# Kernel tuning notes

Measured on AMD Instinct MI355X. Metric: run time of the kernel, lower is better.

Reference implementation:

```python
import jax, jax.numpy as jnp
import numpy as np

H, B, T = 4, 16, 4000
E, D, A, C, K, O = 512, 512, 128, 10, 101, 512


def setup_inputs() -> dict:
    key = jax.random.key(0)
    ks = jax.random.split(key, 12)
    return {
        "enc_pad": jax.random.normal(ks[0], (B, T, E), jnp.float32),
        "enc_len": jax.random.randint(ks[1], (B,), T // 2, T + 1, jnp.int32),
        "dec_z": jax.random.normal(ks[2], (B, D), jnp.float32),
        "att_prev": jax.random.uniform(ks[3], (H, B, T), jnp.float32) / T,
        # learned parameters (per-head stacks)
        "Wenc": jax.random.normal(ks[4], (H, E, A), jnp.float32) / np.sqrt(E).astype(np.float32),
        "benc": jnp.zeros((H, A), jnp.float32),
        "Wdec": jax.random.normal(ks[5], (H, D, A), jnp.float32) / np.sqrt(D).astype(np.float32),
        "Watt": jax.random.normal(ks[6], (H, C, A), jnp.float32) / np.sqrt(C).astype(np.float32),
        "conv_w": jax.random.normal(ks[7], (H, C, K), jnp.float32) / np.sqrt(K).astype(np.float32),
        "gv": jax.random.normal(ks[8], (H, A), jnp.float32) / np.sqrt(A).astype(np.float32),
        "Wo": jax.random.normal(ks[9], (H * E, O), jnp.float32) / np.sqrt(H * E).astype(np.float32),
        "bo": jnp.zeros((O,), jnp.float32),
    }


def reference(enc_pad, enc_len, dec_z, att_prev, Wenc, benc, Wdec, Watt, conv_w, gv, Wo, bo):
    scaling = 1.0
    Hh, Bb, Tt = att_prev.shape
    Cc, Kk = conv_w.shape[1], conv_w.shape[2]
    pad_l = Kk // 2
    pad_r = Kk // 2 if Kk % 2 == 1 else Kk // 2 - 1
    # location conv: grouped 1D conv over heads. lhs [B,H,Tp], rhs [H*C,1,K]
    x = jnp.pad(att_prev.transpose(1, 0, 2), ((0, 0), (0, 0), (pad_l, pad_r)))
    rhs = conv_w.reshape(Hh * Cc, 1, Kk)
    conv = jax.lax.conv_general_dilated(
        x, rhs, window_strides=(1,), padding='VALID',
        dimension_numbers=('NCH', 'OIH', 'NCH'), feature_group_count=Hh)  # [B,H*C,T]
    conv = conv.reshape(Bb, Hh, Cc, Tt)
    att_conv = jnp.einsum('bhct,hca->bhta', conv, Watt)                    # mlp_att
    enc_proj = jnp.einsum('bte,hea->bhta', enc_pad, Wenc) + benc[None, :, None, :]  # mlp_enc
    dec_proj = jnp.einsum('bd,hda->bha', dec_z, Wdec)[:, :, None, :]       # mlp_dec
    e = jnp.einsum('bhta,ha->bht', jnp.tanh(enc_proj + dec_proj + att_conv), gv)  # gvec
    w = jax.nn.softmax(scaling * e, axis=-1)                               # [B,H,T]
    c = jnp.einsum('bht,bte->bhe', w, enc_pad).reshape(Bb, Hh * enc_pad.shape[-1])
    out = c @ Wo + bo                                                      # mlp_o
    return out, w.transpose(1, 0, 2)  # ws stacked as [H,B,T]
```

## Files before the change

kernel.cpp:

```cpp
#include <hip/hip_runtime.h>
#include <hip/hip_bf16.h>

#define H_ 4
#define B_ 16
#define T_ 4000
#define E_ 512
#define D_ 512
#define A_ 128
#define C_ 10
#define K_ 101
#define O_ 512
#define TC_ 50
#define CH_ (T_ / TC_)

typedef __attribute__((ext_vector_type(4))) float f32x4;
typedef __attribute__((ext_vector_type(8)))  short short8;

#define MFMA16(a, b, c) __builtin_amdgcn_mfma_f32_16x16x32_bf16(a, b, c, 0, 0, 0)

#define GLL16(gp, lp) __builtin_amdgcn_global_load_lds( \
    (const __attribute__((address_space(1))) unsigned int*)(gp), \
    (__attribute__((address_space(3))) unsigned int*)(lp), 16, 0, 0)

static __device__ __forceinline__ unsigned short f2bf(float x) {
  unsigned u = __float_as_uint(x);
  unsigned r = (u + 0x7FFFu + ((u >> 16) & 1u)) >> 16;
  return (unsigned short)r;
}
static __device__ __forceinline__ unsigned pk2(float a, float b) {
  return (unsigned)f2bf(a) | ((unsigned)f2bf(b) << 16);
}
static __device__ __forceinline__ unsigned cvtpk(float lo, float hi) {
  unsigned r;
  asm("v_cvt_pk_bf16_f32 %0, %1, %2" : "=v"(r) : "v"(lo), "v"(hi));
  return r;
}
static __device__ __forceinline__ uint4 packbf8(float4 f0, float4 f1) {
  uint4 u;
  u.x = cvtpk(f0.x, f0.y); u.y = cvtpk(f0.z, f0.w);
  u.z = cvtpk(f1.x, f1.y); u.w = cvtpk(f1.z, f1.w);
  return u;
}
static __device__ __forceinline__ float tanh_fast(float x) {
  return 1.0f - 2.0f / (__expf(2.0f * x) + 1.0f);
}
static __device__ __forceinline__ int swz(int r) {
  return (r & 3) ^ ((r >> 2) & 3);
}

__global__ __launch_bounds__(256) void k_prep(const float* __restrict__ Wenc,
                                              const float* __restrict__ Watt,
                                              const float* __restrict__ dec_z,
                                              const float* __restrict__ Wdec,
                                              const float* __restrict__ benc,
                                              char* __restrict__ wbs2,
                                              char* __restrict__ wattb2,
                                              float* __restrict__ addv4) {
  const int bid = blockIdx.x;
  const int tid = threadIdx.x;
  if (bid < 128) {
    const int c = bid * 256 + tid;
    const int kt = c >> 11;
    const int ci = c & 2047;
    const int col = ci >> 2, cc = ci & 3;
    const int h = col >> 7, a = col & 127;
    const int kk = kt * 32 + ((cc ^ swz(col)) & 3) * 8;
    const float* w = Wenc + ((size_t)h * E_ + kk) * A_ + a;
    uint4 u;
    u.x = pk2(w[0], w[A_]);
    u.y = pk2(w[2 * A_], w[3 * A_]);
    u.z = pk2(w[4 * A_], w[5 * A_]);
    u.w = pk2(w[6 * A_], w[7 * A_]);
    ((uint4*)wbs2)[c] = u;
  } else if (bid == 128) {
#pragma unroll
    for (int q = 0; q < 4; ++q) {
      const int cw = q * 256 + tid;
      const int h = cw >> 8;
      const int rr = cw & 255;
      const int col = rr >> 1, half = rr & 1;
      unsigned short v[8];
#pragma unroll
      for (int j = 0; j < 8; ++j) {
        const int k = half * 8 + j;
        v[j] = (k < C_) ? f2bf(Watt[((size_t)h * C_ + k) * A_ + col]) : (unsigned short)0;
      }
      uint4 u;
      u.x = (unsigned)v[0] | ((unsigned)v[1] << 16);
      u.y = (unsigned)v[2] | ((unsigned)v[3] << 16);
      u.z = (unsigned)v[4] | ((unsigned)v[5] << 16);
      u.w = (unsigned)v[6] | ((unsigned)v[7] << 16);
      ((uint4*)wattb2)[cw] = u;
    }
  } else {
    const int idx = bid - 129;
    const int b = idx >> 3, h = (idx >> 1) & 3, ks = idx & 1;
    const int a = tid & 127, kh = tid >> 7;
    const int p = ks * 2 + kh;
    const int d0 = p * 128;
    const float* z = dec_z + (size_t)b * D_ + d0;
    const float* w = Wdec + ((size_t)h * D_ + d0) * A_ + a;
    float s = (p == 0) ? benc[h * A_ + a] : 0.f;
#pragma unroll 8
    for (int d = 0; d < 128; ++d) s += z[d] * w[(size_t)d * A_];
    addv4[(((size_t)p * B_ + b) * H_ + h) * A_ + a] = s;
  }
}

__global__ __launch_bounds__(256) void k_conv(const float* __restrict__ att_prev,
                                              const float* __restrict__ conv_w,
                                              char* __restrict__ convpad) {
  const int bh = blockIdx.x;
  const int b = bh / H_, h = bh % H_;
  const int t0 = blockIdx.y * 256;
  __shared__ float ap[256 + K_ - 1 + 3];
  __shared__ float cw[C_ * K_];
  const float* src = att_prev + ((size_t)h * B_ + b) * T_;
  for (int i = threadIdx.x; i < 256 + K_ - 1; i += 256) {
    int tt = t0 - (K_ / 2) + i;
    ap[i] = (tt >= 0 && tt < T_) ? src[tt] : 0.f;
  }
  for (int i = threadIdx.x; i < C_ * K_; i += 256) cw[i] = conv_w[(size_t)h * C_ * K_ + i];
  __syncthreads();
  const int t = t0 + threadIdx.x;
  if (t < T_) {
    float s[C_];
#pragma unroll
    for (int c = 0; c < C_; ++c) s[c] = 0.f;
    for (int k = 0; k < K_; ++k) {
      float apv = ap[threadIdx.x + k];
#pragma unroll
      for (int c = 0; c < C_; ++c) s[c] += cw[c * K_ + k] * apv;
    }
    uint4 u0, u1;
    u0.x = pk2(s[0], s[1]); u0.y = pk2(s[2], s[3]);
    u0.z = pk2(s[4], s[5]); u0.w = pk2(s[6], s[7]);
    u1.x = pk2(s[8], s[9]); u1.y = 0u; u1.z = 0u; u1.w = 0u;
    char* dst = convpad + (size_t)(b * T_ + t) * 128 + h * 32;
    *(uint4*)dst = u0;
    *(uint4*)(dst + 16) = u1;
  }
}

__global__ __launch_bounds__(512, 4) void k_fused_e_mfma(
    const float* __restrict__ enc,
    const char*  __restrict__ wbs2,
    const char*  __restrict__ convpad,
    const char*  __restrict__ wattb2,
    const float* __restrict__ addv4,
    const float* __restrict__ gv,
    float* __restrict__ e_out) {
  __shared__ char smem[73728];
  const int tid = threadIdx.x;
  const int wv = tid >> 6;
  const int lane = tid & 63, l15 = lane & 15, lg = lane >> 4;
  const int m0 = blockIdx.x * 64;
  const int h = wv >> 1;
  const bool aRole = (wv < 4);

  f32x4 acc[4][4];
#pragma unroll
  for (int i = 0; i < 4; ++i)
#pragma unroll
    for (int j = 0; j < 4; ++j) acc[i][j] = (f32x4){0.f, 0.f, 0.f, 0.f};

  int aOff[4], bOff[4];
#pragma unroll
  for (int q = 0; q < 4; ++q) {
    const int row = q * 16 + l15;
    aOff[q] = row * 64 + (((lg ^ swz(row)) & 3) << 4);
    const int col = wv * 64 + q * 16 + l15;
    bOff[q] = col * 64 + (((lg ^ swz(col)) & 3) << 4);
  }

  const int arow = tid >> 2, ac = tid & 3;
  const int ks = ((ac ^ swz(arow)) & 3) * 8;
  const float* eR = enc + (size_t)(m0 + arow) * E_ + ks;
  const int wOff = arow * 64 + ac * 16;
  const char* bsrc = wbs2 + (size_t)(wv - 4) * 8192 + lane * 16;
  char* bdstBase = smem + 8192 + (wv - 4) * 8192;

  float4 X0, X1;

  if (aRole) {
    float4 c0 = *(const float4*)eR;
    float4 c1 = *(const float4*)(eR + 4);
    X0 = *(const float4*)(eR + 32);
    X1 = *(const float4*)(eR + 36);
    *(uint4*)(smem + wOff) = packbf8(c0, c1);
    asm volatile("s_waitcnt vmcnt(2) lgkmcnt(0)" ::: "memory");
  } else {
#pragma unroll
    for (int i = 0; i < 8; ++i)
      GLL16(bsrc + i * 1024, bdstBase + i * 1024);
    asm volatile("s_waitcnt vmcnt(0) lgkmcnt(0)" ::: "memory");
  }
  __builtin_amdgcn_sched_barrier(0);
  __builtin_amdgcn_s_barrier();

#pragma unroll 1
  for (int kt = 0; kt < 16; ++kt) {
    const int cur = kt & 1;
    const char* bufA = smem + cur * 4096;
    const char* bufB = smem + 8192 + cur * 32768;

    if (!aRole && kt < 15) {
      const char* s = bsrc + (size_t)(kt + 1) * 32768;
      char* d = smem + 8192 + (cur ^ 1) * 32768 + (wv - 4) * 8192;
#pragma unroll
      for (int i = 0; i < 8; ++i)
        GLL16(s + i * 1024, d + i * 1024);
    }
    __builtin_amdgcn_sched_barrier(0);

    short8 aF[4];
#pragma unroll
    for (int q = 0; q < 4; ++q) aF[q] = *(const short8*)(bufA + aOff[q]);
#pragma unroll
    for (int qn = 0; qn < 4; ++qn) {
      short8 bF = *(const short8*)(bufB + bOff[qn]);
#pragma unroll
      for (int qm = 0; qm < 4; ++qm)
        acc[qm][qn] = MFMA16(aF[qm], bF, acc[qm][qn]);
    }

    if (aRole) {
      if (kt < 15)
        *(uint4*)(smem + (cur ^ 1) * 4096 + wOff) = packbf8(X0, X1);
      if (kt < 14) {
        X0 = *(const float4*)(eR + (kt + 2) * 32);
        X1 = *(const float4*)(eR + (kt + 2) * 32 + 4);
      }
    }

    if (kt < 14) {
      if (aRole)
        asm volatile("s_waitcnt vmcnt(2) lgkmcnt(0)" ::: "memory");
      else
        asm volatile("s_waitcnt vmcnt(0) lgkmcnt(0)" ::: "memory");
    } else {
      asm volatile("s_waitcnt vmcnt(0) lgkmcnt(0)" ::: "memory");
    }
    __builtin_amdgcn_sched_barrier(0);
    __builtin_amdgcn_s_barrier();
  }

  {
    short8 zf;
#pragma unroll
    for (int i = 0; i < 8; ++i) zf[i] = 0;
    short8 cf[4], wf[4];
#pragma unroll
    for (int q = 0; q < 4; ++q) { cf[q] = zf; wf[q] = zf; }
    if (lg < 2) {
#pragma unroll
      for (int q = 0; q < 4; ++q) {
        const int row = m0 + q * 16 + l15;
        cf[q] = *(const short8*)(convpad + (size_t)row * 128 + h * 32 + lg * 16);
        const int col = (wv & 1) * 64 + q * 16 + l15;
        wf[q] = *(const short8*)(wattb2 + ((size_t)h * 128 + col) * 32 + lg * 16);
      }
    }
#pragma unroll
    for (int qm = 0; qm < 4; ++qm)
#pragma unroll
      for (int qn = 0; qn < 4; ++qn)
        acc[qm][qn] = MFMA16(cf[qm], wf[qn], acc[qm][qn]);
  }

  {
    const unsigned b0w = (unsigned)m0 / 4000u;
    const unsigned b1w = (unsigned)(m0 + 63) / 4000u;
    float av0[4], av1[4], gvr[4];
#pragma unroll
    for (int qn = 0; qn < 4; ++qn) {
      const int col = (wv & 1) * 64 + qn * 16 + l15;
      const int i0 = (int)b0w * 512 + h * 128 + col;
      const int i1 = (int)b1w * 512 + h * 128 + col;
      av0[qn] = addv4[i0] + addv4[8192 + i0] + addv4[16384 + i0] + addv4[24576 + i0];
      av1[qn] = addv4[i1] + addv4[8192 + i1] + addv4[16384 + i1] + addv4[24576 + i1];
      gvr[qn] = gv[h * 128 + col];
    }
    float* Pb = (float*)smem;
#pragma unroll
    for (int qm = 0; qm < 4; ++qm) {
#pragma unroll
      for (int r = 0; r < 4; ++r) {
        const int rowLocal = qm * 16 + lg * 4 + r;
        const unsigned brow = (unsigned)(m0 + rowLocal);
        const unsigned bb = brow / 4000u;
        const int sel = (bb != b0w);
        float s = 0.f;
#pragma unroll
        for (int qn = 0; qn < 4; ++qn)
          s += gvr[qn] * tanh_fast(acc[qm][qn][r] + (sel ? av1[qn] : av0[qn]));
        s += __shfl_xor(s, 1);
        s += __shfl_xor(s, 2);
        s += __shfl_xor(s, 4);
        s += __shfl_xor(s, 8);
        if (l15 == 0) Pb[wv * 64 + rowLocal] = s;
      }
    }
  }
  __syncthreads();
  if (tid < 256) {
    const float* Pb = (const float*)smem;
    const int hh = tid >> 6, r = tid & 63;
    const float ev = Pb[(hh * 2) * 64 + r] + Pb[(hh * 2 + 1) * 64 + r];
    const unsigned brow = (unsigned)(m0 + r);
    const unsigned bb = brow / 4000u;
    const unsigned tt = brow - bb * 4000u;
    e_out[((size_t)bb * H_ + hh) * T_ + tt] = ev;
  }
}

__global__ __launch_bounds__(256) void k_msum(const float* __restrict__ e_in,
                                              float2* __restrict__ msum) {
  const int bh = blockIdx.x;
  const float* er = e_in + (size_t)bh * T_;
  __shared__ float red[256];
  const int tid = threadIdx.x;
  float m = -1e30f;
  for (int t = tid; t < T_; t += 256) m = fmaxf(m, er[t]);
  red[tid] = m;
  __syncthreads();
  for (int s = 128; s > 0; s >>= 1) {
    if (tid < s) red[tid] = fmaxf(red[tid], red[tid + s]);
    __syncthreads();
  }
  m = red[0];
  __syncthreads();
  float sum = 0.f;
  for (int t = tid; t < T_; t += 256) sum += __expf(er[t] - m);
  red[tid] = sum;
  __syncthreads();
  for (int s = 128; s > 0; s >>= 1) {
    if (tid < s) red[tid] += red[tid + s];
    __syncthreads();
  }
  if (tid == 0) msum[bh] = make_float2(m, 1.0f / red[0]);
}

__global__ __launch_bounds__(128) void k_ctx(const float* __restrict__ enc,
                                             const float* __restrict__ e_in,
                                             const float2* __restrict__ msum,
                                             float* __restrict__ wout,
                                             float* __restrict__ partial) {
  const int b = blockIdx.x, tc = blockIdx.y;
  const int t0 = tc * CH_;
  const int tid = threadIdx.x;
  __shared__ float wls[H_ * CH_];
  for (int i = tid; i < H_ * CH_; i += 128) {
    const int h = i / CH_, tt = i - h * CH_;
    const float2 ms = msum[b * H_ + h];
    const float w = __expf(e_in[((size_t)b * H_ + h) * T_ + t0 + tt] - ms.x) * ms.y;
    wls[i] = w;
    wout[((size_t)h * B_ + b) * T_ + t0 + tt] = w;
  }
  __syncthreads();
  float4 a0 = {0,0,0,0}, a1 = {0,0,0,0}, a2 = {0,0,0,0}, a3 = {0,0,0,0};
  const float4* enc4 = (const float4*)enc;
  const size_t ebase = ((size_t)b * T_ + t0) * 128 + tid;
#pragma unroll 8
  for (int tt = 0; tt < CH_; ++tt) {
    const float4 x = enc4[ebase + (size_t)tt * 128];
    const float w0 = wls[tt], w1 = wls[CH_ + tt], w2 = wls[2 * CH_ + tt], w3 = wls[3 * CH_ + tt];
    a0.x += w0 * x.x; a0.y += w0 * x.y; a0.z += w0 * x.z; a0.w += w0 * x.w;
    a1.x += w1 * x.x; a1.y += w1 * x.y; a1.z += w1 * x.z; a1.w += w1 * x.w;
    a2.x += w2 * x.x; a2.y += w2 * x.y; a2.z += w2 * x.z; a2.w += w2 * x.w;
    a3.x += w3 * x.x; a3.y += w3 * x.y; a3.z += w3 * x.z; a3.w += w3 * x.w;
  }
  float4* p4 = (float4*)partial;
  const size_t pbase = (((size_t)tc * B_ + b) * H_) * 128 + tid;
  p4[pbase] = a0;
  p4[pbase + 128] = a1;
  p4[pbase + 256] = a2;
  p4[pbase + 384] = a3;
}

__global__ __launch_bounds__(256) void k_out_part(const float* __restrict__ partial,
                                                  const float* __restrict__ Wo,
                                                  float* __restrict__ p2) {
  const int b = blockIdx.x;
  const int o = blockIdx.y * 256 + threadIdx.x;
  const int kc = blockIdx.z;
  __shared__ float cS[256];
  const int he0 = kc * 256;
  {
    float s = 0.f;
#pragma unroll
    for (int tc = 0; tc < TC_; ++tc)
      s += partial[((size_t)tc * B_ + b) * (H_ * E_) + he0 + threadIdx.x];
    cS[threadIdx.x] = s;
  }
  __syncthreads();
  float s = 0.f;
#pragma unroll 8
  for (int i = 0; i < 256; ++i) s += cS[i] * Wo[(size_t)(he0 + i) * O_ + o];
  p2[((size_t)kc * B_ + b) * O_ + o] = s;
}

__global__ __launch_bounds__(512) void k_out_fin(const float* __restrict__ p2,
                                                 const float* __restrict__ bo,
                                                 float* __restrict__ out) {
  const int b = blockIdx.x, o = threadIdx.x;
  float s = bo[o];
#pragma unroll
  for (int kc = 0; kc < 8; ++kc) s += p2[((size_t)kc * B_ + b) * O_ + o];
  out[b * O_ + o] = s;
}

extern "C" void kernel_launch(void* const* d_in, const int* in_sizes, int n_in,
                              void* d_out, int out_size, void* d_ws, size_t ws_size,
                              hipStream_t stream) {
  (void)in_sizes; (void)n_in; (void)out_size; (void)ws_size;
  const float* enc      = (const float*)d_in[0];
  const float* dec_z    = (const float*)d_in[2];
  const float* att_prev = (const float*)d_in[3];
  const float* Wenc     = (const float*)d_in[4];
  const float* benc     = (const float*)d_in[5];
  const float* Wdec     = (const float*)d_in[6];
  const float* Watt     = (const float*)d_in[7];
  const float* conv_w   = (const float*)d_in[8];
  const float* gv       = (const float*)d_in[9];
  const float* Wo       = (const float*)d_in[10];
  const float* bo       = (const float*)d_in[11];

  float* out  = (float*)d_out;
  float* wout = out + B_ * O_;

  char* wsb = (char*)d_ws;
  float*  e_buf   = (float*)(wsb);
  char*   convpad = wsb + 1024000;
  char*   wbs2    = wsb + 9216000;
  char*   wattb2  = wsb + 9740288;
  float*  addv4   = (float*)(wsb + 9756672);
  float2* msum    = (float2*)(wsb + 9887744);
  float*  partial = (float*)(wsb + 9888256);
  float*  p2      = (float*)(wsb + 16441856);

  hipLaunchKernelGGL(k_prep, dim3(257), dim3(256), 0, stream,
                     Wenc, Watt, dec_z, Wdec, benc, wbs2, wattb2, addv4);
  hipLaunchKernelGGL(k_conv, dim3(B_ * H_, 16), dim3(256), 0, stream, att_prev, conv_w, convpad);
  hipLaunchKernelGGL(k_fused_e_mfma, dim3(1000), dim3(512), 0, stream,
                     enc, wbs2, convpad, wattb2, addv4, gv, e_buf);
  hipLaunchKernelGGL(k_msum, dim3(B_ * H_), dim3(256), 0, stream, e_buf, msum);
  hipLaunchKernelGGL(k_ctx, dim3(B_, TC_), dim3(128), 0, stream, enc, e_buf, msum, wout, partial);
  hipLaunchKernelGGL(k_out_part, dim3(B_, O_ / 256, 8), dim3(256), 0, stream, partial, Wo, p2);
  hipLaunchKernelGGL(k_out_fin, dim3(B_), dim3(512), 0, stream, p2, bo, out);
}
```

Baseline: 143.2 us.

## Split k_ctx time chunk across four warps, add MFMA priority and pointer increments

k_ctx now launches 512 threads per block. Four groups of 128 each cover 20 of the 80 timesteps in the chunk, and their accumulators are combined through shared memory before the partial is written. The aim is more loads in flight and better occupancy on the bandwidth-bound context pass over enc. The MFMA GEMM loop also gains s_setprio around its MFMA block and replaces recomputed prefetch addresses with incremented pointers. The cost is a shared-memory reduction and an extra barrier in k_ctx.

```diff
diff --git a/kernel.cpp b/kernel.cpp
--- a/kernel.cpp
+++ b/kernel.cpp
@@ -181,6 +181,8 @@
   char* bdstBase = smem + 8192 + (wv - 4) * 8192;
 
   float4 X0, X1;
+  const float* eP = eR + 64;
+  const char* bsP = bsrc + 32768;
 
   if (aRole) {
     float4 c0 = *(const float4*)eR;
@@ -205,17 +207,17 @@
     const char* bufB = smem + 8192 + cur * 32768;
 
     if (!aRole && kt < 15) {
-      const char* s = bsrc + (size_t)(kt + 1) * 32768;
       char* d = smem + 8192 + (cur ^ 1) * 32768 + (wv - 4) * 8192;
 #pragma unroll
       for (int i = 0; i < 8; ++i)
-        GLL16(s + i * 1024, d + i * 1024);
+        GLL16(bsP + i * 1024, d + i * 1024);
     }
     __builtin_amdgcn_sched_barrier(0);
 
     short8 aF[4];
 #pragma unroll
     for (int q = 0; q < 4; ++q) aF[q] = *(const short8*)(bufA + aOff[q]);
+    __builtin_amdgcn_s_setprio(1);
 #pragma unroll
     for (int qn = 0; qn < 4; ++qn) {
       short8 bF = *(const short8*)(bufB + bOff[qn]);
@@ -223,14 +225,18 @@
       for (int qm = 0; qm < 4; ++qm)
         acc[qm][qn] = MFMA16(aF[qm], bF, acc[qm][qn]);
     }
+    __builtin_amdgcn_s_setprio(0);
 
     if (aRole) {
       if (kt < 15)
         *(uint4*)(smem + (cur ^ 1) * 4096 + wOff) = packbf8(X0, X1);
       if (kt < 14) {
-        X0 = *(const float4*)(eR + (kt + 2) * 32);
-        X1 = *(const float4*)(eR + (kt + 2) * 32 + 4);
+        X0 = *(const float4*)eP;
+        X1 = *(const float4*)(eP + 4);
+        eP += 32;
       }
+    } else {
+      bsP += 32768;
     }
 
     if (kt < 14) {
@@ -341,7 +347,7 @@
   if (tid == 0) msum[bh] = make_float2(m, 1.0f / red[0]);
 }
 
-__global__ __launch_bounds__(128) void k_ctx(const float* __restrict__ enc,
+__global__ __launch_bounds__(512) void k_ctx(const float* __restrict__ enc,
                                              const float* __restrict__ e_in,
                                              const float2* __restrict__ msum,
                                              float* __restrict__ wout,
@@ -349,8 +355,10 @@
   const int b = blockIdx.x, tc = blockIdx.y;
   const int t0 = tc * CH_;
   const int tid = threadIdx.x;
+  const int grp = tid >> 7, lt = tid & 127;
   __shared__ float wls[H_ * CH_];
-  for (int i = tid; i < H_ * CH_; i += 128) {
+  __shared__ float4 red[3][4][128];
+  for (int i = tid; i < H_ * CH_; i += 512) {
     const int h = i / CH_, tt = i - h * CH_;
     const float2 ms = msum[b * H_ + h];
     const float w = __expf(e_in[((size_t)b * H_ + h) * T_ + t0 + tt] - ms.x) * ms.y;
@@ -360,22 +368,44 @@
   __syncthreads();
   float4 a0 = {0,0,0,0}, a1 = {0,0,0,0}, a2 = {0,0,0,0}, a3 = {0,0,0,0};
   const float4* enc4 = (const float4*)enc;
-  const size_t ebase = ((size_t)b * T_ + t0) * 128 + tid;
-#pragma unroll 8
-  for (int tt = 0; tt < CH_; ++tt) {
+  const int tg = grp * 20;
+  const size_t ebase = ((size_t)b * T_ + t0 + tg) * 128 + lt;
+#pragma unroll 5
+  for (int tt = 0; tt < 20; ++tt) {
     const float4 x = enc4[ebase + (size_t)tt * 128];
-    const float w0 = wls[tt], w1 = wls[CH_ + tt], w2 = wls[2 * CH_ + tt], w3 = wls[3 * CH_ + tt];
+    const float w0 = wls[tg + tt];
+    const float w1 = wls[CH_ + tg + tt];
+    const float w2 = wls[2 * CH_ + tg + tt];
+    const float w3 = wls[3 * CH_ + tg + tt];
     a0.x += w0 * x.x; a0.y += w0 * x.y; a0.z += w0 * x.z; a0.w += w0 * x.w;
     a1.x += w1 * x.x; a1.y += w1 * x.y; a1.z += w1 * x.z; a1.w += w1 * x.w;
     a2.x += w2 * x.x; a2.y += w2 * x.y; a2.z += w2 * x.z; a2.w += w2 * x.w;
     a3.x += w3 * x.x; a3.y += w3 * x.y; a3.z += w3 * x.z; a3.w += w3 * x.w;
   }
-  float4* p4 = (float4*)partial;
-  const size_t pbase = (((size_t)tc * B_ + b) * H_) * 128 + tid;
-  p4[pbase] = a0;
-  p4[pbase + 128] = a1;
-  p4[pbase + 256] = a2;
-  p4[pbase + 384] = a3;
+  if (grp > 0) {
+    red[grp - 1][0][lt] = a0;
+    red[grp - 1][1][lt] = a1;
+    red[grp - 1][2][lt] = a2;
+    red[grp - 1][3][lt] = a3;
+  }
+  __syncthreads();
+  if (grp == 0) {
+#pragma unroll
+    for (int g = 0; g < 3; ++g) {
+      const float4 r0 = red[g][0][lt], r1 = red[g][1][lt];
+      const float4 r2 = red[g][2][lt], r3 = red[g][3][lt];
+      a0.x += r0.x; a0.y += r0.y; a0.z += r0.z; a0.w += r0.w;
+      a1.x += r1.x; a1.y += r1.y; a1.z += r1.z; a1.w += r1.w;
+      a2.x += r2.x; a2.y += r2.y; a2.z += r2.z; a2.w += r2.w;
+      a3.x += r3.x; a3.y += r3.y; a3.z += r3.z; a3.w += r3.w;
+    }
+    float4* p4 = (float4*)partial;
+    const size_t pbase = (((size_t)tc * B_ + b) * H_) * 128 + lt;
+    p4[pbase] = a0;
+    p4[pbase + 128] = a1;
+    p4[pbase + 256] = a2;
+    p4[pbase + 384] = a3;
+  }
 }
 
 __global__ __launch_bounds__(256) void k_out_part(const float* __restrict__ partial,
@@ -445,7 +475,7 @@
   hipLaunchKernelGGL(k_fused_e_mfma, dim3(1000), dim3(512), 0, stream,
                      enc, wbs2, convpad, wattb2, addv4, gv, e_buf);
   hipLaunchKernelGGL(k_msum, dim3(B_ * H_), dim3(256), 0, stream, e_buf, msum);
-  hipLaunchKernelGGL(k_ctx, dim3(B_, TC_), dim3(128), 0, stream, enc, e_buf, msum, wout, partial);
+  hipLaunchKernelGGL(k_ctx, dim3(B_, TC_), dim3(512), 0, stream, enc, e_buf, msum, wout, partial);
   hipLaunchKernelGGL(k_out_part, dim3(B_, O_ / 256, 8), dim3(256), 0, stream, partial, Wo, p2);
   hipLaunchKernelGGL(k_out_fin, dim3(B_), dim3(512), 0, stream, p2, bo, out);
 }
```

New measurement: 143.4 us. Within noise of the previous version (+0.1%).
